# Kernel tuning notes

Measured on AMD Instinct MI355X. Metric: run time of the kernel, lower is better.

## Reference

```python
import jax, jax.numpy as jnp
import numpy as np
from jax import lax

_GRAY = jnp.array([0.299, 0.587, 0.114], dtype=jnp.float32)  # cv2 RGB2GRAY weights


def _conv(x, w, b):
    # x: [B,C,H,W], w: [O,I,kh,kw], SAME padding (matches padding=k//2 for odd k)
    y = lax.conv_general_dilated(x, w, (1, 1), 'SAME',
                                 dimension_numbers=('NCHW', 'OIHW', 'NCHW'))
    return y + b[None, :, None, None]


def _maxpool2(x):
    return lax.reduce_window(x, -jnp.inf, lax.max, (1, 1, 2, 2), (1, 1, 2, 2), 'VALID')


def _resize_bilinear(img, out_h, out_w):
    # cv2.resize INTER_LINEAR semantics: half-pixel-centered bilinear sampling, edge clamped
    B, C, H, W = img.shape
    ys = jnp.clip((jnp.arange(out_h, dtype=jnp.float32) + 0.5) * (H / out_h) - 0.5, 0.0, H - 1)
    xs = jnp.clip((jnp.arange(out_w, dtype=jnp.float32) + 0.5) * (W / out_w) - 0.5, 0.0, W - 1)
    y0 = jnp.floor(ys).astype(jnp.int32)
    x0 = jnp.floor(xs).astype(jnp.int32)
    y1 = jnp.minimum(y0 + 1, H - 1)
    x1 = jnp.minimum(x0 + 1, W - 1)
    wy = (ys - y0.astype(jnp.float32))[None, None, :, None]
    wx = (xs - x0.astype(jnp.float32))[None, None, None, :]
    r0 = img[:, :, y0, :]
    r1 = img[:, :, y1, :]
    rows = r0 * (1.0 - wy) + r1 * wy          # [B,C,out_h,W]
    c0 = rows[:, :, :, x0]
    c1 = rows[:, :, :, x1]
    return c0 * (1.0 - wx) + c1 * wx          # [B,C,out_h,out_w]


def _forward(input, w1, b1, w2, b2, w3, b3, w4, b4, w5, b5):
    x = jax.nn.relu(_conv(input, w1, b1))
    x = _maxpool2(x)
    x = jax.nn.relu(_conv(x, w2, b2))
    x = _maxpool2(x)
    x = jax.nn.relu(_conv(x, w3, b3))
    x = jax.nn.relu(_conv(x, w4, b4))
    x = _conv(x, w5, b5)                       # [B,1,H/4,W/4]
    out_h, out_w = x.shape[2], x.shape[3]
    # rgb2gray path is detached in the original (detach().cpu()): stop_gradient
    gray = jnp.einsum('bchw,c->bhw', lax.stop_gradient(input), _GRAY)[:, None]  # [B,1,H,W]
    gray = _resize_bilinear(gray, out_h, out_w)
    return jax.nn.relu(x + jax.nn.relu(gray))


def setup_inputs() -> dict:
    key = jax.random.key(0)
    ks = jax.random.split(key, 12)
    B, H, W = 8, 768, 1024
    def w(k, shape, fan_in):
        return (jax.random.normal(k, shape, dtype=jnp.float32) / np.sqrt(fan_in)).astype(jnp.float32)
    return {
        'input': jax.random.normal(ks[0], (B, 3, H, W), dtype=jnp.float32),
        'w1': w(ks[1], (20, 3, 7, 7), 3 * 49),  'b1': jnp.zeros((20,), jnp.float32),
        'w2': w(ks[2], (40, 20, 5, 5), 20 * 25), 'b2': jnp.zeros((40,), jnp.float32),
        'w3': w(ks[3], (20, 40, 5, 5), 40 * 25), 'b3': jnp.zeros((20,), jnp.float32),
        'w4': w(ks[4], (10, 20, 5, 5), 20 * 25), 'b4': jnp.zeros((10,), jnp.float32),
        'w5': w(ks[5], (1, 10, 1, 1), 10),       'b5': jnp.zeros((1,), jnp.float32),
    }


def reference(input, w1, b1, w2, b2, w3, b3, w4, b4, w5, b5):
    return _forward(input, w1, b1, w2, b2, w3, b3, w4, b4, w5, b5)
```

## Files before the change

### kernel.cpp

```cpp
#include <hip/hip_runtime.h>


typedef _Float16 half_t;
typedef _Float16 half8 __attribute__((ext_vector_type(8)));
typedef float floatx4 __attribute__((ext_vector_type(4)));

#define IN_H 768
#define IN_W 1024
#define P1H 384
#define P1W 512
#define P2H 192
#define P2W 256

#define OFF_P2 0ULL
#define OFF_P1 44040192ULL
#define OFF_X3 44040192ULL
#define OFF_W2 119537664ULL
#define OFF_W3 119599104ULL
#define OFF_W4 119803904ULL
#define OFF_W1 119824384ULL

union PK4 { half_t h[4]; uint2 u; };
union U8 { half8 v; uint2 u[2]; };

__global__ __launch_bounds__(256) void pack_weights(
    const float* __restrict__ w2, const float* __restrict__ w3,
    const float* __restrict__ w4, const float* __restrict__ w1,
    half_t* __restrict__ wp2, half_t* __restrict__ wp3, half_t* __restrict__ wp4,
    half_t* __restrict__ wp1)
{
  int t = blockIdx.x * 256 + threadIdx.x;
  if (t < 30720) {
    int ky = t / 6144, r = t % 6144;
    int kk = r / 1536, r2 = r % 1536, oc = r2 >> 5, k = r2 & 31;
    int o = kk * 32 + k, p = o / 24, c = o % 24;
    float v = (oc < 40 && c < 20 && p < 5) ? w2[(oc * 20 + c) * 25 + ky * 5 + p] : 0.f;
    wp2[t] = (half_t)v;
  } else if (t < 81920) {
    int u = t - 30720;
    int tap = u / 2048, r = u % 2048, oc = r >> 6, c = r & 63;
    float v = (oc < 20 && c < 40) ? w3[(oc * 40 + c) * 25 + tap] : 0.f;
    wp3[u] = (half_t)v;
  } else if (t < 92160) {
    int u = t - 81920;
    int ky = u / 2048, r = u % 2048;
    int kk = r / 512, r2 = r % 512, oc = r2 >> 5, k = r2 & 31;
    int o = kk * 32 + k, p = o / 24, c = o % 24;
    float v = (oc < 10 && c < 20 && p < 5) ? w4[(oc * 20 + c) * 25 + ky * 5 + p] : 0.f;
    wp4[u] = (half_t)v;
  } else if (t < 99328) {
    int u = t - 92160;
    int ky = u / 1024, r = u % 1024, oc = r >> 5, k = r & 31;
    int kx = k >> 2, c = k & 3;
    float v = (oc < 20 && c < 3 && kx < 7) ? w1[((oc * 3 + c) * 7 + ky) * 7 + kx] : 0.f;
    wp1[u] = (half_t)v;
  }
}

__global__ __launch_bounds__(256) void conv1_mfma(
    const float* __restrict__ in, const half_t* __restrict__ wp,
    const float* __restrict__ bias, half_t* __restrict__ P1)
{
  __shared__ __align__(16) half_t ltile[38 * 40 * 4];
  const int b = blockIdx.z, ty0 = blockIdx.y * 32, tx0 = blockIdx.x * 32;
  const int tid = threadIdx.x;
  const int HW1 = IN_H * IN_W;

  const float* p0 = in + (size_t)b * 3 * HW1;
  const bool interior = (blockIdx.x >= 1) && (blockIdx.x <= 30) &&
                        (blockIdx.y >= 1) && (blockIdx.y <= 22);
  if (interior) {
    for (int i = tid; i < 380; i += 256) {
      int r = i / 10, c4 = i - r * 10;
      const float* pr = p0 + (size_t)(ty0 - 3 + r) * IN_W + (tx0 - 4 + 4 * c4);
      float4 v0 = *(const float4*)(pr);
      float4 v1 = *(const float4*)(pr + HW1);
      float4 v2 = *(const float4*)(pr + 2 * HW1);
      PK4 a0, a1, a2, a3;
      a0.h[0] = (half_t)v0.x; a0.h[1] = (half_t)v1.x; a0.h[2] = (half_t)v2.x; a0.h[3] = (half_t)0.f;
      a1.h[0] = (half_t)v0.y; a1.h[1] = (half_t)v1.y; a1.h[2] = (half_t)v2.y; a1.h[3] = (half_t)0.f;
      a2.h[0] = (half_t)v0.z; a2.h[1] = (half_t)v1.z; a2.h[2] = (half_t)v2.z; a2.h[3] = (half_t)0.f;
      a3.h[0] = (half_t)v0.w; a3.h[1] = (half_t)v1.w; a3.h[2] = (half_t)v2.w; a3.h[3] = (half_t)0.f;
      uint4* dst = (uint4*)(ltile + (r * 40 + 4 * c4) * 4);
      dst[0] = make_uint4(a0.u.x, a0.u.y, a1.u.x, a1.u.y);
      dst[1] = make_uint4(a2.u.x, a2.u.y, a3.u.x, a3.u.y);
    }
  } else {
    for (int i = tid; i < 1520; i += 256) {
      int r = i / 40, c = i - r * 40;
      int gy = ty0 - 3 + r, gx = tx0 - 4 + c;
      float v0 = 0.f, v1 = 0.f, v2 = 0.f;
      if (gy >= 0 && gy < IN_H && (unsigned)gx < (unsigned)IN_W) {
        size_t o = (size_t)gy * IN_W + gx;
        v0 = p0[o];
        v1 = p0[o + HW1];
        v2 = p0[o + 2 * HW1];
      }
      PK4 pk;
      pk.h[0] = (half_t)v0; pk.h[1] = (half_t)v1;
      pk.h[2] = (half_t)v2; pk.h[3] = (half_t)0.f;
      *(uint2*)(ltile + (r * 40 + c) * 4) = pk.u;
    }
  }
  __syncthreads();

  const int wv = tid >> 6, ln = tid & 63, q = ln >> 4, nl = ln & 15;
  const int cbase = (2 * nl + 2 * q + 1) * 4;
  const half_t* wA = wp + nl * 32 + q * 8;

  floatx4 bv[2];
  #pragma unroll
  for (int mt = 0; mt < 2; ++mt)
    #pragma unroll
    for (int r = 0; r < 4; ++r) {
      int oc = mt * 16 + q * 4 + r;
      bv[mt][r] = (oc < 20) ? bias[oc] : 0.f;
    }
  const int pc = (tx0 >> 1) + nl;

  #pragma unroll
  for (int p = 0; p < 2; ++p) {
    const int rbase = p * 16 + 4 * wv;
    U8 frag[4][2];
    #pragma unroll
    for (int d = 0; d < 4; ++d) {
      const half_t* rp = ltile + (rbase + d) * 160 + cbase;
      #pragma unroll
      for (int phx = 0; phx < 2; ++phx) {
        frag[d][phx].u[0] = *(const uint2*)(rp + phx * 4);
        frag[d][phx].u[1] = *(const uint2*)(rp + phx * 4 + 4);
      }
    }
    half8 Abuf[2][2];
    Abuf[0][0] = *(const half8*)(wA);
    Abuf[0][1] = *(const half8*)(wA + 512);
    floatx4 acc[2][8];
    #pragma unroll
    for (int mt = 0; mt < 2; ++mt)
      #pragma unroll
      for (int j = 0; j < 8; ++j) acc[mt][j] = (floatx4){0.f, 0.f, 0.f, 0.f};

    #pragma unroll
    for (int ky = 0; ky < 7; ++ky) {
      if (ky < 6) {
        Abuf[(ky + 1) & 1][0] = *(const half8*)(wA + (ky + 1) * 1024);
        Abuf[(ky + 1) & 1][1] = *(const half8*)(wA + (ky + 1) * 1024 + 512);
      }
      #pragma unroll
      for (int j = 0; j < 8; ++j) {
        const int g = j >> 2, ph = j & 3, phy = ph >> 1, phx = ph & 1;
        half8 B = frag[(2 * g + phy + ky) & 3][phx].v;
        acc[0][j] = __builtin_amdgcn_mfma_f32_16x16x32_f16(Abuf[ky & 1][0], B, acc[0][j], 0, 0, 0);
        acc[1][j] = __builtin_amdgcn_mfma_f32_16x16x32_f16(Abuf[ky & 1][1], B, acc[1][j], 0, 0, 0);
      }
      if (ky < 6) {
        const half_t* rp = ltile + (rbase + ky + 4) * 160 + cbase;
        #pragma unroll
        for (int phx = 0; phx < 2; ++phx) {
          frag[ky & 3][phx].u[0] = *(const uint2*)(rp + phx * 4);
          frag[ky & 3][phx].u[1] = *(const uint2*)(rp + phx * 4 + 4);
        }
      }
    }

    const int pr0 = (ty0 >> 1) + 8 * p + 2 * wv;
    #pragma unroll
    for (int g = 0; g < 2; ++g) {
      size_t pxbase = (((size_t)b * P1H + pr0 + g) * P1W + pc) * 24;
      PK4 pk0;
      #pragma unroll
      for (int r = 0; r < 4; ++r) {
        float x = fmaxf(fmaxf(acc[0][g * 4 + 0][r], acc[0][g * 4 + 1][r]),
                        fmaxf(acc[0][g * 4 + 2][r], acc[0][g * 4 + 3][r]));
        pk0.h[r] = (half_t)fmaxf(x + bv[0][r], 0.f);
      }
      *(uint2*)(P1 + pxbase + q * 4) = pk0.u;
      if (q < 2) {
        PK4 pk1;
        #pragma unroll
        for (int r = 0; r < 4; ++r) {
          float x = fmaxf(fmaxf(acc[1][g * 4 + 0][r], acc[1][g * 4 + 1][r]),
                          fmaxf(acc[1][g * 4 + 2][r], acc[1][g * 4 + 3][r]));
          pk1.h[r] = (half_t)fmaxf(x + bv[1][r], 0.f);
        }
        *(uint2*)(P1 + pxbase + 16 + q * 4) = pk1.u;
      }
    }
  }
}

__global__ __launch_bounds__(256, 2) void conv2_mfma(
    const half_t* __restrict__ P1, const half_t* __restrict__ wp,
    const float* __restrict__ bias, half_t* __restrict__ P2)
{
  __shared__ __align__(16) half_t lin[20 * 36 * 24 + 16];
  const int b = blockIdx.z, ty0 = blockIdx.y * 16, tx0 = blockIdx.x * 32;
  const int tid = threadIdx.x;
  if (tid < 16) lin[20 * 36 * 24 + tid] = (half_t)0.f;
  for (int i = tid; i < 2160; i += 256) {
    int px = i / 3, part = i - px * 3;
    int row = px / 36, col = px - row * 36;
    int gy = ty0 - 2 + row, gx = tx0 - 2 + col;
    uint4 v = make_uint4(0, 0, 0, 0);
    if (gy >= 0 && gy < P1H && (unsigned)gx < (unsigned)P1W)
      v = *(const uint4*)(P1 + (((size_t)b * P1H + gy) * P1W + gx) * 24 + part * 8);
    *(uint4*)(lin + px * 24 + part * 8) = v;
  }
  __syncthreads();

  const int wv = tid >> 6, ln = tid & 63, q = ln >> 4, nl = ln & 15;
  const half_t* cb0 = lin + 2 * nl * 24 + q * 8;
  const half_t* wA = wp + nl * 32 + q * 8;

  floatx4 acc[3][8];
  #pragma unroll
  for (int mt = 0; mt < 3; ++mt)
    #pragma unroll
    for (int j = 0; j < 8; ++j) acc[mt][j] = (floatx4){0.f, 0.f, 0.f, 0.f};

  #pragma unroll
  for (int ky = 0; ky < 5; ++ky) {
    #pragma unroll
    for (int kk = 0; kk < 4; ++kk) {
      const half_t* wt = wA + (ky * 4 + kk) * 1536;
      half8 A0 = *(const half8*)(wt);
      half8 A1 = *(const half8*)(wt + 512);
      half8 A2 = *(const half8*)(wt + 1024);
      #pragma unroll
      for (int j = 0; j < 8; ++j) {
        const int g = j >> 2, phy = (j >> 1) & 1, phx = j & 1;
        half8 B = *(const half8*)(cb0 + (4 * wv + 2 * g + phy + ky) * 864 + phx * 24 + kk * 32);
        acc[0][j] = __builtin_amdgcn_mfma_f32_16x16x32_f16(A0, B, acc[0][j], 0, 0, 0);
        acc[1][j] = __builtin_amdgcn_mfma_f32_16x16x32_f16(A1, B, acc[1][j], 0, 0, 0);
        acc[2][j] = __builtin_amdgcn_mfma_f32_16x16x32_f16(A2, B, acc[2][j], 0, 0, 0);
      }
    }
  }

  floatx4 bv[3];
  #pragma unroll
  for (int mt = 0; mt < 3; ++mt)
    #pragma unroll
    for (int r = 0; r < 4; ++r) {
      int oc = mt * 16 + q * 4 + r;
      bv[mt][r] = (oc < 40) ? bias[oc] : 0.f;
    }
  const int pr0 = (ty0 >> 1) + 2 * wv;
  const int pc = (tx0 >> 1) + nl;
  #pragma unroll
  for (int g = 0; g < 2; ++g) {
    size_t pxbase = (((size_t)b * P2H + pr0 + g) * P2W + pc) * 56;
    #pragma unroll
    for (int mt = 0; mt < 3; ++mt) {
      PK4 pk;
      #pragma unroll
      for (int r = 0; r < 4; ++r) {
        float x = fmaxf(fmaxf(acc[mt][g * 4 + 0][r], acc[mt][g * 4 + 1][r]),
                        fmaxf(acc[mt][g * 4 + 2][r], acc[mt][g * 4 + 3][r]));
        pk.h[r] = (half_t)fmaxf(x + bv[mt][r], 0.f);
      }
      *(uint2*)(P2 + pxbase + mt * 16 + q * 4) = pk.u;
    }
    if (q == 0)
      *(uint4*)(P2 + pxbase + 48) = make_uint4(0, 0, 0, 0);
  }
}

__global__ __launch_bounds__(256, 2) void conv3_mfma(
    const half_t* __restrict__ P2, const half_t* __restrict__ wp,
    const float* __restrict__ bias, half_t* __restrict__ X3)
{
  __shared__ __align__(16) half_t lin[12 * 36 * 56 + 16];
  const int b = blockIdx.z, ty0 = blockIdx.y * 8, tx0 = blockIdx.x * 32;
  const int tid = threadIdx.x;
  if (tid < 16) lin[12 * 36 * 56 + tid] = (half_t)0.f;
  for (int i = tid; i < 3024; i += 256) {
    int px = i / 7, part = i - px * 7;
    int row = px / 36, col = px - row * 36;
    int gy = ty0 - 2 + row, gx = tx0 - 2 + col;
    uint4 v = make_uint4(0, 0, 0, 0);
    if (gy >= 0 && gy < P2H && (unsigned)gx < (unsigned)P2W)
      v = *(const uint4*)(P2 + (((size_t)b * P2H + gy) * P2W + gx) * 56 + part * 8);
    *(uint4*)(lin + px * 56 + part * 8) = v;
  }
  __syncthreads();

  const int wv = tid >> 6, ln = tid & 63, q = ln >> 4, nl = ln & 15;
  const int cbase = 2 * nl * 56 + q * 8;
  half8 frag[2][6][2];
  #pragma unroll
  for (int c = 0; c < 6; ++c)
    #pragma unroll
    for (int cb = 0; cb < 2; ++cb) {
      frag[0][c][cb] = *(const half8*)(lin + (2 * wv + 0) * 2016 + cbase + c * 56 + cb * 32);
      frag[1][c][cb] = *(const half8*)(lin + (2 * wv + 1) * 2016 + cbase + c * 56 + cb * 32);
    }
  const half_t* wA = wp + nl * 64 + q * 8;
  half8 Abuf[2][2][2];
  #pragma unroll
  for (int mt = 0; mt < 2; ++mt)
    #pragma unroll
    for (int cb = 0; cb < 2; ++cb)
      Abuf[0][mt][cb] = *(const half8*)(wA + mt * 1024 + cb * 32);
  floatx4 acc[2][4];
  #pragma unroll
  for (int mt = 0; mt < 2; ++mt)
    #pragma unroll
    for (int j = 0; j < 4; ++j) acc[mt][j] = (floatx4){0.f, 0.f, 0.f, 0.f};

  #pragma unroll
  for (int ky = 0; ky < 5; ++ky) {
    #pragma unroll
    for (int kx = 0; kx < 5; ++kx) {
      const int tap = ky * 5 + kx;
      if (tap < 24) {
        #pragma unroll
        for (int mt = 0; mt < 2; ++mt)
          #pragma unroll
          for (int cb = 0; cb < 2; ++cb)
            Abuf[(tap + 1) & 1][mt][cb] =
                *(const half8*)(wA + (tap + 1) * 2048 + mt * 1024 + cb * 32);
      }
      #pragma unroll
      for (int cb = 0; cb < 2; ++cb)
        #pragma unroll
        for (int j = 0; j < 4; ++j) {
          const int phy = j >> 1, phx = j & 1;
          half8 B = frag[(ky + phy) & 1][kx + phx][cb];
          acc[0][j] = __builtin_amdgcn_mfma_f32_16x16x32_f16(Abuf[tap & 1][0][cb], B, acc[0][j], 0, 0, 0);
          acc[1][j] = __builtin_amdgcn_mfma_f32_16x16x32_f16(Abuf[tap & 1][1][cb], B, acc[1][j], 0, 0, 0);
        }
    }
    if (ky < 4) {
      const half_t* rp = lin + (2 * wv + ky + 2) * 2016 + cbase;
      #pragma unroll
      for (int c = 0; c < 6; ++c)
        #pragma unroll
        for (int cb = 0; cb < 2; ++cb)
          frag[ky & 1][c][cb] = *(const half8*)(rp + c * 56 + cb * 32);
    }
  }

  floatx4 bv[2];
  #pragma unroll
  for (int mt = 0; mt < 2; ++mt)
    #pragma unroll
    for (int r = 0; r < 4; ++r) {
      int oc = mt * 16 + q * 4 + r;
      bv[mt][r] = (oc < 20) ? bias[oc] : 0.f;
    }
  #pragma unroll
  for (int j = 0; j < 4; ++j) {
    const int phy = j >> 1, phx = j & 1;
    int y = ty0 + 2 * wv + phy, x = tx0 + 2 * nl + phx;
    size_t pxbase = (((size_t)b * P2H + y) * P2W + x) * 24;
    #pragma unroll
    for (int mt = 0; mt < 2; ++mt) {
      if (mt == 1 && q >= 2) continue;
      floatx4 v = acc[mt][j];
      PK4 pk;
      #pragma unroll
      for (int r = 0; r < 4; ++r) pk.h[r] = (half_t)fmaxf(v[r] + bv[mt][r], 0.f);
      *(uint2*)(X3 + pxbase + mt * 16 + q * 4) = pk.u;
    }
  }
}

__global__ __launch_bounds__(256, 2) void conv4_mfma(
    const half_t* __restrict__ X3, const half_t* __restrict__ wp,
    const float* __restrict__ bias, const float* __restrict__ w5,
    const float* __restrict__ b5, const float* __restrict__ in,
    float* __restrict__ out)
{
  __shared__ __align__(16) half_t lin[20 * 36 * 24 + 16];
  const int b = blockIdx.z, ty0 = blockIdx.y * 16, tx0 = blockIdx.x * 32;
  const int tid = threadIdx.x;
  if (tid < 16) lin[20 * 36 * 24 + tid] = (half_t)0.f;
  for (int i = tid; i < 2160; i += 256) {
    int px = i / 3, part = i - px * 3;
    int row = px / 36, col = px - row * 36;
    int gy = ty0 - 2 + row, gx = tx0 - 2 + col;
    uint4 v = make_uint4(0, 0, 0, 0);
    if (gy >= 0 && gy < P2H && (unsigned)gx < (unsigned)P2W)
      v = *(const uint4*)(X3 + (((size_t)b * P2H + gy) * P2W + gx) * 24 + part * 8);
    *(uint4*)(lin + px * 24 + part * 8) = v;
  }
  __syncthreads();

  const int wv = tid >> 6, ln = tid & 63, q = ln >> 4, nl = ln & 15;
  const half_t* cb0 = lin + 2 * nl * 24 + q * 8;
  const half_t* wA = wp + nl * 32 + q * 8;

  floatx4 acc[8];
  #pragma unroll
  for (int j = 0; j < 8; ++j) acc[j] = (floatx4){0.f, 0.f, 0.f, 0.f};

  #pragma unroll
  for (int ky = 0; ky < 5; ++ky) {
    #pragma unroll
    for (int kk = 0; kk < 4; ++kk) {
      half8 A = *(const half8*)(wA + (ky * 4 + kk) * 512);
      #pragma unroll
      for (int j = 0; j < 8; ++j) {
        const int g = j >> 2, phy = (j >> 1) & 1, phx = j & 1;
        half8 B = *(const half8*)(cb0 + (4 * wv + 2 * g + phy + ky) * 864 + phx * 24 + kk * 32);
        acc[j] = __builtin_amdgcn_mfma_f32_16x16x32_f16(A, B, acc[j], 0, 0, 0);
      }
    }
  }

  float bv[4], w5v[4];
  #pragma unroll
  for (int r = 0; r < 4; ++r) {
    int oc = q * 4 + r;
    bv[r]  = (oc < 10) ? bias[oc] : 0.f;
    w5v[r] = (oc < 10) ? w5[oc] : 0.f;
  }
  const float b5v = b5[0];
  const float* inb = in + (size_t)b * 3 * (IN_H * IN_W);

  #pragma unroll
  for (int g = 0; g < 2; ++g)
    #pragma unroll
    for (int phy = 0; phy < 2; ++phy) {
      const int y = ty0 + 4 * wv + 2 * g + phy;
      const int x0 = tx0 + 2 * nl;
      float s0 = 0.f, s1 = 0.f;
      #pragma unroll
      for (int r = 0; r < 4; ++r) {
        s0 += w5v[r] * fmaxf(acc[g * 4 + 2 * phy + 0][r] + bv[r], 0.f);
        s1 += w5v[r] * fmaxf(acc[g * 4 + 2 * phy + 1][r] + bv[r], 0.f);
      }
      s0 += __shfl_xor(s0, 16); s0 += __shfl_xor(s0, 32);
      s1 += __shfl_xor(s1, 16); s1 += __shfl_xor(s1, 32);
      if (q == 0) {
        const size_t cb = (size_t)(4 * y + 1) * IN_W + 4 * x0;
        float g0 = 0.f, g1 = 0.f;
        #pragma unroll
        for (int ch = 0; ch < 3; ++ch) {
          const float coef = (ch == 0) ? 0.299f : ((ch == 1) ? 0.587f : 0.114f);
          const float* qp = inb + (size_t)ch * (IN_H * IN_W);
          float4 a0 = *(const float4*)(qp + cb);
          float4 a1 = *(const float4*)(qp + cb + 4);
          float4 d0 = *(const float4*)(qp + cb + IN_W);
          float4 d1 = *(const float4*)(qp + cb + IN_W + 4);
          g0 += coef * (a0.y + a0.z + d0.y + d0.z);
          g1 += coef * (a1.y + a1.z + d1.y + d1.z);
        }
        float o0 = fmaxf(s0 + b5v + fmaxf(g0 * 0.25f, 0.f), 0.f);
        float o1 = fmaxf(s1 + b5v + fmaxf(g1 * 0.25f, 0.f), 0.f);
        *(float2*)(out + ((size_t)b * P2H + y) * P2W + x0) = make_float2(o0, o1);
      }
    }
}

extern "C" void kernel_launch(void* const* d_in, const int* in_sizes, int n_in,
                              void* d_out, int out_size, void* d_ws, size_t ws_size,
                              hipStream_t stream) {
  const float* input = (const float*)d_in[0];
  const float* w1 = (const float*)d_in[1];  const float* b1 = (const float*)d_in[2];
  const float* w2 = (const float*)d_in[3];  const float* b2 = (const float*)d_in[4];
  const float* w3 = (const float*)d_in[5];  const float* b3 = (const float*)d_in[6];
  const float* w4 = (const float*)d_in[7];  const float* b4 = (const float*)d_in[8];
  const float* w5 = (const float*)d_in[9];  const float* b5 = (const float*)d_in[10];
  float* out = (float*)d_out;
  char* ws = (char*)d_ws;

  half_t* P2h = (half_t*)(ws + OFF_P2);
  half_t* P1h = (half_t*)(ws + OFF_P1);
  half_t* X3h = (half_t*)(ws + OFF_X3);
  half_t* wp2 = (half_t*)(ws + OFF_W2);
  half_t* wp3 = (half_t*)(ws + OFF_W3);
  half_t* wp4 = (half_t*)(ws + OFF_W4);
  half_t* wp1 = (half_t*)(ws + OFF_W1);

  pack_weights<<<388, 256, 0, stream>>>(w2, w3, w4, w1, wp2, wp3, wp4, wp1);
  conv1_mfma<<<dim3(32, 24, 8), 256, 0, stream>>>(input, wp1, b1, P1h);
  conv2_mfma<<<dim3(16, 24, 8), 256, 0, stream>>>(P1h, wp2, b2, P2h);
  conv3_mfma<<<dim3(8, 24, 8), 256, 0, stream>>>(P2h, wp3, b3, X3h);
  conv4_mfma<<<dim3(8, 12, 8), 256, 0, stream>>>(X3h, wp4, b4, w5, b5, input, out);
}
```

Measured before the change: 365.2 us.

## Shrink P2 stride to 48 channels and fold conv3 taps into packed K

The pooled conv2 output P2 is stored with 48 instead of 56 half channels per pixel, and the zero-fill of the padding tail is dropped. This cuts P2 write/read traffic and conv3 LDS footprint. Conv3 now packs the kx taps and channels of each kernel row into a contiguous K dimension of 240 padded to 256, which removes the padded 64-channel slots per tap and the double-buffered fragment scheme. Operands are loaded directly from LDS and global memory per K step, giving fewer MFMAs at the cost of more LDS loads. The conv1 interior staging also switches from float4 to float2 loads with more iterations.

```diff
diff --git a/kernel.cpp b/kernel.cpp
--- a/kernel.cpp
+++ b/kernel.cpp
@@ -17,8 +17,8 @@
 #define OFF_X3 44040192ULL
 #define OFF_W2 119537664ULL
 #define OFF_W3 119599104ULL
-#define OFF_W4 119803904ULL
-#define OFF_W1 119824384ULL
+#define OFF_W4 119681024ULL
+#define OFF_W1 119701504ULL
 
 union PK4 { half_t h[4]; uint2 u; };
 union U8 { half8 v; uint2 u[2]; };
@@ -36,20 +36,22 @@
     int o = kk * 32 + k, p = o / 24, c = o % 24;
     float v = (oc < 40 && c < 20 && p < 5) ? w2[(oc * 20 + c) * 25 + ky * 5 + p] : 0.f;
     wp2[t] = (half_t)v;
+  } else if (t < 71680) {
+    int u = t - 30720;
+    int ky = u / 8192, r = u % 8192;
+    int kk = r / 1024, r2 = r % 1024, oc = r2 >> 5, k = r2 & 31;
+    int o = kk * 32 + k, p = o / 48, c = o % 48;
+    float v = (oc < 20 && c < 40 && p < 5) ? w3[(oc * 40 + c) * 25 + ky * 5 + p] : 0.f;
+    wp3[u] = (half_t)v;
   } else if (t < 81920) {
-    int u = t - 30720;
-    int tap = u / 2048, r = u % 2048, oc = r >> 6, c = r & 63;
-    float v = (oc < 20 && c < 40) ? w3[(oc * 40 + c) * 25 + tap] : 0.f;
-    wp3[u] = (half_t)v;
-  } else if (t < 92160) {
-    int u = t - 81920;
+    int u = t - 71680;
     int ky = u / 2048, r = u % 2048;
     int kk = r / 512, r2 = r % 512, oc = r2 >> 5, k = r2 & 31;
     int o = kk * 32 + k, p = o / 24, c = o % 24;
     float v = (oc < 10 && c < 20 && p < 5) ? w4[(oc * 20 + c) * 25 + ky * 5 + p] : 0.f;
     wp4[u] = (half_t)v;
-  } else if (t < 99328) {
-    int u = t - 92160;
+  } else if (t < 89088) {
+    int u = t - 81920;
     int ky = u / 1024, r = u % 1024, oc = r >> 5, k = r & 31;
     int kx = k >> 2, c = k & 3;
     float v = (oc < 20 && c < 3 && kx < 7) ? w1[((oc * 3 + c) * 7 + ky) * 7 + kx] : 0.f;
@@ -70,20 +72,17 @@
   const bool interior = (blockIdx.x >= 1) && (blockIdx.x <= 30) &&
                         (blockIdx.y >= 1) && (blockIdx.y <= 22);
   if (interior) {
-    for (int i = tid; i < 380; i += 256) {
-      int r = i / 10, c4 = i - r * 10;
-      const float* pr = p0 + (size_t)(ty0 - 3 + r) * IN_W + (tx0 - 4 + 4 * c4);
-      float4 v0 = *(const float4*)(pr);
-      float4 v1 = *(const float4*)(pr + HW1);
-      float4 v2 = *(const float4*)(pr + 2 * HW1);
-      PK4 a0, a1, a2, a3;
+    for (int i = tid; i < 760; i += 256) {
+      int r = i / 20, c2 = i - r * 20;
+      const float* pr = p0 + (size_t)(ty0 - 3 + r) * IN_W + (tx0 - 4 + 2 * c2);
+      float2 v0 = *(const float2*)(pr);
+      float2 v1 = *(const float2*)(pr + HW1);
+      float2 v2 = *(const float2*)(pr + 2 * HW1);
+      PK4 a0, a1;
       a0.h[0] = (half_t)v0.x; a0.h[1] = (half_t)v1.x; a0.h[2] = (half_t)v2.x; a0.h[3] = (half_t)0.f;
       a1.h[0] = (half_t)v0.y; a1.h[1] = (half_t)v1.y; a1.h[2] = (half_t)v2.y; a1.h[3] = (half_t)0.f;
-      a2.h[0] = (half_t)v0.z; a2.h[1] = (half_t)v1.z; a2.h[2] = (half_t)v2.z; a2.h[3] = (half_t)0.f;
-      a3.h[0] = (half_t)v0.w; a3.h[1] = (half_t)v1.w; a3.h[2] = (half_t)v2.w; a3.h[3] = (half_t)0.f;
-      uint4* dst = (uint4*)(ltile + (r * 40 + 4 * c4) * 4);
-      dst[0] = make_uint4(a0.u.x, a0.u.y, a1.u.x, a1.u.y);
-      dst[1] = make_uint4(a2.u.x, a2.u.y, a3.u.x, a3.u.y);
+      *(uint4*)(ltile + (r * 40 + 2 * c2) * 4) =
+          make_uint4(a0.u.x, a0.u.y, a1.u.x, a1.u.y);
     }
   } else {
     for (int i = tid; i < 1520; i += 256) {
@@ -249,7 +248,7 @@
   const int pc = (tx0 >> 1) + nl;
   #pragma unroll
   for (int g = 0; g < 2; ++g) {
-    size_t pxbase = (((size_t)b * P2H + pr0 + g) * P2W + pc) * 56;
+    size_t pxbase = (((size_t)b * P2H + pr0 + g) * P2W + pc) * 48;
     #pragma unroll
     for (int mt = 0; mt < 3; ++mt) {
       PK4 pk;
@@ -261,8 +260,6 @@
       }
       *(uint2*)(P2 + pxbase + mt * 16 + q * 4) = pk.u;
     }
-    if (q == 0)
-      *(uint4*)(P2 + pxbase + 48) = make_uint4(0, 0, 0, 0);
   }
 }
 
@@ -270,74 +267,45 @@
     const half_t* __restrict__ P2, const half_t* __restrict__ wp,
     const float* __restrict__ bias, half_t* __restrict__ X3)
 {
-  __shared__ __align__(16) half_t lin[12 * 36 * 56 + 16];
+  __shared__ __align__(16) half_t lin[12 * 36 * 48 + 16];
   const int b = blockIdx.z, ty0 = blockIdx.y * 8, tx0 = blockIdx.x * 32;
   const int tid = threadIdx.x;
-  if (tid < 16) lin[12 * 36 * 56 + tid] = (half_t)0.f;
-  for (int i = tid; i < 3024; i += 256) {
-    int px = i / 7, part = i - px * 7;
+  if (tid < 16) lin[12 * 36 * 48 + tid] = (half_t)0.f;
+  for (int i = tid; i < 2592; i += 256) {
+    int px = i / 6, part = i - px * 6;
     int row = px / 36, col = px - row * 36;
     int gy = ty0 - 2 + row, gx = tx0 - 2 + col;
     uint4 v = make_uint4(0, 0, 0, 0);
     if (gy >= 0 && gy < P2H && (unsigned)gx < (unsigned)P2W)
-      v = *(const uint4*)(P2 + (((size_t)b * P2H + gy) * P2W + gx) * 56 + part * 8);
-    *(uint4*)(lin + px * 56 + part * 8) = v;
+      v = *(const uint4*)(P2 + (((size_t)b * P2H + gy) * P2W + gx) * 48 + part * 8);
+    *(uint4*)(lin + px * 48 + part * 8) = v;
   }
   __syncthreads();
 
   const int wv = tid >> 6, ln = tid & 63, q = ln >> 4, nl = ln & 15;
-  const int cbase = 2 * nl * 56 + q * 8;
-  half8 frag[2][6][2];
-  #pragma unroll
-  for (int c = 0; c < 6; ++c)
-    #pragma unroll
-    for (int cb = 0; cb < 2; ++cb) {
-      frag[0][c][cb] = *(const half8*)(lin + (2 * wv + 0) * 2016 + cbase + c * 56 + cb * 32);
-      frag[1][c][cb] = *(const half8*)(lin + (2 * wv + 1) * 2016 + cbase + c * 56 + cb * 32);
-    }
-  const half_t* wA = wp + nl * 64 + q * 8;
-  half8 Abuf[2][2][2];
+  const half_t* cb0 = lin + 2 * nl * 48 + q * 8;
+  const half_t* wA = wp + nl * 32 + q * 8;
+
+  floatx4 acc[2][4];
   #pragma unroll
   for (int mt = 0; mt < 2; ++mt)
     #pragma unroll
-    for (int cb = 0; cb < 2; ++cb)
-      Abuf[0][mt][cb] = *(const half8*)(wA + mt * 1024 + cb * 32);
-  floatx4 acc[2][4];
-  #pragma unroll
-  for (int mt = 0; mt < 2; ++mt)
-    #pragma unroll
     for (int j = 0; j < 4; ++j) acc[mt][j] = (floatx4){0.f, 0.f, 0.f, 0.f};
 
   #pragma unroll
   for (int ky = 0; ky < 5; ++ky) {
     #pragma unroll
-    for (int kx = 0; kx < 5; ++kx) {
-      const int tap = ky * 5 + kx;
-      if (tap < 24) {
-        #pragma unroll
-        for (int mt = 0; mt < 2; ++mt)
-          #pragma unroll
-          for (int cb = 0; cb < 2; ++cb)
-            Abuf[(tap + 1) & 1][mt][cb] =
-                *(const half8*)(wA + (tap + 1) * 2048 + mt * 1024 + cb * 32);
-      }
-      #pragma unroll
-      for (int cb = 0; cb < 2; ++cb)
-        #pragma unroll
-        for (int j = 0; j < 4; ++j) {
-          const int phy = j >> 1, phx = j & 1;
-          half8 B = frag[(ky + phy) & 1][kx + phx][cb];
-          acc[0][j] = __builtin_amdgcn_mfma_f32_16x16x32_f16(Abuf[tap & 1][0][cb], B, acc[0][j], 0, 0, 0);
-          acc[1][j] = __builtin_amdgcn_mfma_f32_16x16x32_f16(Abuf[tap & 1][1][cb], B, acc[1][j], 0, 0, 0);
-        }
-    }
-    if (ky < 4) {
-      const half_t* rp = lin + (2 * wv + ky + 2) * 2016 + cbase;
-      #pragma unroll
-      for (int c = 0; c < 6; ++c)
-        #pragma unroll
-        for (int cb = 0; cb < 2; ++cb)
-          frag[ky & 1][c][cb] = *(const half8*)(rp + c * 56 + cb * 32);
+    for (int kk = 0; kk < 8; ++kk) {
+      const half_t* wt = wA + (ky * 8 + kk) * 1024;
+      half8 A0 = *(const half8*)(wt);
+      half8 A1 = *(const half8*)(wt + 512);
+      #pragma unroll
+      for (int j = 0; j < 4; ++j) {
+        const int phy = j >> 1, phx = j & 1;
+        half8 B = *(const half8*)(cb0 + (2 * wv + phy + ky) * 1728 + phx * 48 + kk * 32);
+        acc[0][j] = __builtin_amdgcn_mfma_f32_16x16x32_f16(A0, B, acc[0][j], 0, 0, 0);
+        acc[1][j] = __builtin_amdgcn_mfma_f32_16x16x32_f16(A1, B, acc[1][j], 0, 0, 0);
+      }
     }
   }
 
@@ -474,7 +442,7 @@
   half_t* wp4 = (half_t*)(ws + OFF_W4);
   half_t* wp1 = (half_t*)(ws + OFF_W1);
 
-  pack_weights<<<388, 256, 0, stream>>>(w2, w3, w4, w1, wp2, wp3, wp4, wp1);
+  pack_weights<<<348, 256, 0, stream>>>(w2, w3, w4, w1, wp2, wp3, wp4, wp1);
   conv1_mfma<<<dim3(32, 24, 8), 256, 0, stream>>>(input, wp1, b1, P1h);
   conv2_mfma<<<dim3(16, 24, 8), 256, 0, stream>>>(P1h, wp2, b2, P2h);
   conv3_mfma<<<dim3(8, 24, 8), 256, 0, stream>>>(P2h, wp3, b3, X3h);
```

New measurement: 329.2 us. 1.11x faster.
